# Kernel optimization log

Hardware: AMD Instinct MI355X
Metric: run time of the kernel (lower is better)

## Reference

```python
import jax, jax.numpy as jnp
import numpy as np

# Constants from mode='only_tv': gamma_l1=gamma_dwt=beta=lambda_l1=lambda_dwt=sigma=0,
# so u_l1,u_dwt,z,eta_l1,eta_dwt,rho stay identically zero and drop out of the math.
GAMMA_TV = 2.0
ALPHA = 5.0
LAMBDA_TV = 1e-4
N_ITER = 200


def soft_thresh(v, t):
    return jnp.sign(v) * jnp.maximum(jnp.abs(v) - t, 0.0)


def setup_inputs() -> dict:
    key = jax.random.key(0)
    k1, k2, k3 = jax.random.split(key, 3)
    target = jax.random.normal(k1, (4096, 64), dtype=jnp.float32)  # B spectra of K bands
    A = jax.random.normal(k2, (9, 64), dtype=jnp.float32) * 0.1     # (M=9 channels, K=64 bands)
    x0 = jax.random.normal(k3, (4096, 64), dtype=jnp.float32)       # replaces randn_like(target)
    return {"target": target, "A": A, "x0": x0}


def reference(target, A, x0):
    # target, x0: (B, K) batch of per-sample length-K vectors; A: (M, K)
    K = A.shape[1]
    AT = A.T  # (K, M)
    I = jnp.eye(K, dtype=A.dtype)
    Delta = jnp.roll(I, 1, axis=1) - I          # (K, K)
    DtD = Delta.T @ Delta
    inv_item = jnp.linalg.inv(AT @ A + GAMMA_TV * DtD + ALPHA * I)  # (K, K)

    # b = A @ x  per sample  ->  (B, M);  AT @ b per sample -> (B, K)
    b = target @ A.T
    ATb = b @ A

    # per-sample Delta @ v, batched over rows -> v_mat @ Delta.T
    def D(v):
        return v @ Delta.T

    eta_tv0 = jnp.zeros_like(x0)
    tau0 = jnp.zeros_like(x0)

    def step(carry, _):
        x, eta_tv, tau = carry
        u_tv = soft_thresh(D(x) + eta_tv / GAMMA_TV, LAMBDA_TV / GAMMA_TV)
        w = jnp.maximum(x + tau / ALPHA, 0.0)
        # note: torch's matmul(z_tv, DeltaT) on a vector equals Delta @ z_tv -> batched D(.)
        resid = ATb + D(GAMMA_TV * u_tv - eta_tv) + ALPHA * w - tau
        x = resid @ inv_item.T  # per-sample inv_item @ resid
        eta_tv = eta_tv + GAMMA_TV * (D(x) - u_tv)
        tau = tau + ALPHA * (x - w)
        return (x, eta_tv, tau), None

    (x, _, _), _ = jax.lax.scan(step, (x0, eta_tv0, tau0), None, length=N_ITER)
    return x
```

## Files before the change

### kernel.cpp

```cpp
#include <hip/hip_runtime.h>

#define NSAMP 4096
#define NITER 200

#define DPL(op, acc, rr, mm, rot) \
  op " " acc ", " rr ", " mm " row_ror:" #rot " row_mask:0xf bank_mask:0xf\n\t"

__global__ __launch_bounds__(256)
void admm_fused(const float* __restrict__ target, const float* __restrict__ A,
                const float* __restrict__ x0, float* __restrict__ out) {
  __shared__ __align__(16) char smem[39952];
  float (*Mfull)[64] = (float(*)[64])(smem);
  float* Mperm       = (float*)(smem + 16384);
  float (*rbuf)[64]  = (float(*)[64])(smem + 32768);
  double* lamr       = (double*)(smem + 32768);
  float* binv        = (float*)(smem + 33792);
  float (*P)[64]     = (float(*)[64])(smem + 34048);
  float (*Q)[64]     = (float(*)[64])(smem + 36352);
  double (*W)[18]    = (double(*)[18])(smem + 38656);

  const int tid = threadIdx.x;
  const int wid = tid >> 6;
  const int lane = tid & 63;
  const int s = blockIdx.x * 4 + wid;
  const double TWO_PI = 6.283185307179586476925286766559;

  double cb = 0.0;
  if (tid < 64) {
    cb = cos(TWO_PI * (double)tid / 64.0);
    lamr[tid] = 1.0 / (9.0 - 4.0 * cb);
  }
  __syncthreads();
  if (tid < 64) {
    double cm1 = 1.0, c0 = cb;
    double acc = lamr[0] + cb * lamr[1];
#pragma unroll 16
    for (int m = 2; m < 64; ++m) {
      double c = 2.0 * cb * c0 - cm1;
      cm1 = c0;
      c0 = c;
      acc += c * lamr[m];
    }
    binv[tid] = (float)(acc / 64.0);
  }
  __syncthreads();

  for (int e = tid; e < 9 * 64; e += 256) {
    int m = e >> 6, i = e & 63;
    double acc = 0.0;
#pragma unroll 16
    for (int k = 0; k < 64; ++k)
      acc += (double)A[m * 64 + k] * (double)binv[(k - i) & 63];
    P[m][i] = (float)acc;
  }
  __syncthreads();

  if (tid < 81) {
    int m = tid / 9, n = tid % 9;
    double acc = (m == n) ? 1.0 : 0.0;
#pragma unroll 16
    for (int i = 0; i < 64; ++i)
      acc += (double)P[m][i] * (double)A[n * 64 + i];
    W[m][n] = acc;
    W[m][n + 9] = (m == n) ? 1.0 : 0.0;
  }
  __syncthreads();

  {
    const int r9 = tid / 18, c9 = tid % 18;
    const bool act = (tid < 162);
    for (int k = 0; k < 9; ++k) {
      double pv = 1.0, f = 0.0, wkc = 0.0;
      if (act) {
        pv = W[k][k];
        f = W[r9][k];
        wkc = W[k][c9];
      }
      __syncthreads();
      if (act) {
        double nk = wkc / pv;
        W[r9][c9] = (r9 == k) ? nk : fma(-f, nk, W[r9][c9]);
      }
      __syncthreads();
    }
  }

  for (int e = tid; e < 9 * 64; e += 256) {
    int m = e >> 6, j = e & 63;
    double acc = 0.0;
#pragma unroll
    for (int n = 0; n < 9; ++n) acc += W[m][n + 9] * (double)P[n][j];
    Q[m][j] = (float)acc;
  }
  __syncthreads();

  for (int e = tid; e < 64 * 64; e += 256) {
    int i = e >> 6, j = e & 63;
    float acc = binv[(i - j) & 63];
#pragma unroll
    for (int m = 0; m < 9; ++m) acc = fmaf(-P[m][i], Q[m][j], acc);
    Mfull[i][j] = acc;
  }
  __syncthreads();

  int dpp1;
  asm volatile(
      "s_nop 4\n\t"
      "v_mov_b32_dpp %0, %1 row_ror:1 row_mask:0xf bank_mask:0xf\n\t"
      "s_nop 4"
      : "=v"(dpp1)
      : "v"(lane));
  const int dir = (__builtin_amdgcn_readfirstlane(dpp1) == 1) ? 1 : -1;

  for (int e = tid; e < 64 * 64; e += 256) {
    int li = e >> 6, k = e & 63;
    int j;
    if (k < 32) {
      int t = k & 15;
      int q = (li & 48) | (((li & 15) + dir * t + 16) & 15);
      j = (k < 16) ? q : (q ^ 16);
    } else {
      j = ((li & 32) ^ 32) + (k - 32);
    }
    Mperm[li * 64 + k] = Mfull[li][j];
  }
  __syncthreads();

  float t = target[s * 64 + lane];
  float atbv = 0.f;
#pragma unroll
  for (int m = 0; m < 9; ++m) {
    float a = A[m * 64 + lane];
    float p = t * a;
#pragma unroll
    for (int off = 32; off; off >>= 1) p += __shfl_xor(p, off, 64);
    atbv = fmaf(a, p, atbv);
  }

  unsigned int mprm = (unsigned int)(uintptr_t)(Mperm + lane * 64);
  unsigned int rb = (unsigned int)(uintptr_t)(&rbuf[wid][0]);
  unsigned int a_w = rb + lane * 4;
  unsigned int a_rf = rb + (((lane & 32) ^ 32) << 2);
  unsigned int a_nxt = ((lane + 1) & 63) * 4;
  float xin = x0[s * 64 + lane];
  float xout;
  int cnt_s;
  const int smask = 0x7fffffff;
  const float sthr = 5e-5f, sc02 = 0.2f, sc5 = 5.0f;

  asm volatile(
      "s_mov_b32 m0, -1\n\t"
      "ds_read_b128 v[64:67],   %[mprm]\n\t"
      "ds_read_b128 v[68:71],   %[mprm] offset:16\n\t"
      "ds_read_b128 v[72:75],   %[mprm] offset:32\n\t"
      "ds_read_b128 v[76:79],   %[mprm] offset:48\n\t"
      "ds_read_b128 v[80:83],   %[mprm] offset:64\n\t"
      "ds_read_b128 v[84:87],   %[mprm] offset:80\n\t"
      "ds_read_b128 v[88:91],   %[mprm] offset:96\n\t"
      "ds_read_b128 v[92:95],   %[mprm] offset:112\n\t"
      "ds_read_b128 v[96:99],   %[mprm] offset:128\n\t"
      "ds_read_b128 v[100:103], %[mprm] offset:144\n\t"
      "ds_read_b128 v[104:107], %[mprm] offset:160\n\t"
      "ds_read_b128 v[108:111], %[mprm] offset:176\n\t"
      "ds_read_b128 v[112:115], %[mprm] offset:192\n\t"
      "ds_read_b128 v[116:119], %[mprm] offset:208\n\t"
      "ds_read_b128 v[120:123], %[mprm] offset:224\n\t"
      "ds_read_b128 v[124:127], %[mprm] offset:240\n\t"
      "v_mov_b32 v32, %[xin]\n\t"
      "v_mov_b32 v36, %[atb]\n\t"
      "v_mov_b32 v33, 0\n\t"
      "v_mov_b32 v34, 0\n\t"
      "ds_bpermute_b32 v45, %[anx], v32\n\t"
      "s_waitcnt lgkmcnt(0)\n\t"
      "v_sub_f32 v35, v45, v32\n\t"
      "s_movk_i32 %[cnt], 200\n\t"
      "1:\n\t"
      "v_fma_f32 v40, 0.5, v33, v35\n\t"
      "v_and_b32 v41, %[msk], v40\n\t"
      "v_subrev_f32 v41, %[thr], v41\n\t"
      "v_max_f32 v41, 0, v41\n\t"
      "v_bfi_b32 v42, %[msk], v41, v40\n\t"
      "v_fma_f32 v43, %[c02], v34, v32\n\t"
      "v_max_f32 v43, 0, v43\n\t"
      "v_fma_f32 v40, 2.0, v42, -v33\n\t"
      "ds_bpermute_b32 v45, %[anx], v40\n\t"
      "v_fma_f32 v44, %[c5], v43, v36\n\t"
      "v_sub_f32 v44, v44, v34\n\t"
      "v_sub_f32 v44, v44, v40\n\t"
      "s_waitcnt lgkmcnt(0)\n\t"
      "v_add_f32 v44, v44, v45\n\t"
      "ds_write_b32 %[aw], v44\n\t"
      "ds_swizzle_b32 v47, v44 offset:0x401F\n\t"
      "ds_read_b128 v[48:51], %[arf]\n\t"
      "ds_read_b128 v[52:55], %[arf] offset:16\n\t"
      "ds_read_b128 v[56:59], %[arf] offset:32\n\t"
      "ds_read_b128 v[60:63], %[arf] offset:48\n\t"
      "ds_read_b128 v[16:19], %[arf] offset:64\n\t"
      "ds_read_b128 v[20:23], %[arf] offset:80\n\t"
      "ds_read_b128 v[24:27], %[arf] offset:96\n\t"
      "ds_read_b128 v[28:31], %[arf] offset:112\n\t"
      "v_mul_f32 v37, v44, v64\n\t"
      DPL("v_mul_f32",  "v38", "v44", "v65", 1)
      DPL("v_mul_f32",  "v39", "v44", "v66", 2)
      DPL("v_mul_f32",  "v40", "v44", "v67", 3)
      DPL("v_fmac_f32", "v37", "v44", "v68", 4)
      DPL("v_fmac_f32", "v38", "v44", "v69", 5)
      DPL("v_fmac_f32", "v39", "v44", "v70", 6)
      DPL("v_fmac_f32", "v40", "v44", "v71", 7)
      DPL("v_fmac_f32", "v37", "v44", "v72", 8)
      DPL("v_fmac_f32", "v38", "v44", "v73", 9)
      DPL("v_fmac_f32", "v39", "v44", "v74", 10)
      DPL("v_fmac_f32", "v40", "v44", "v75", 11)
      DPL("v_fmac_f32", "v37", "v44", "v76", 12)
      DPL("v_fmac_f32", "v38", "v44", "v77", 13)
      DPL("v_fmac_f32", "v39", "v44", "v78", 14)
      DPL("v_fmac_f32", "v40", "v44", "v79", 15)
      "s_waitcnt lgkmcnt(8)\n\t"
      "s_nop 1\n\t"
      "v_fmac_f32 v37, v47, v80\n\t"
      DPL("v_fmac_f32", "v38", "v47", "v81", 1)
      DPL("v_fmac_f32", "v39", "v47", "v82", 2)
      DPL("v_fmac_f32", "v40", "v47", "v83", 3)
      DPL("v_fmac_f32", "v37", "v47", "v84", 4)
      DPL("v_fmac_f32", "v38", "v47", "v85", 5)
      DPL("v_fmac_f32", "v39", "v47", "v86", 6)
      DPL("v_fmac_f32", "v40", "v47", "v87", 7)
      DPL("v_fmac_f32", "v37", "v47", "v88", 8)
      DPL("v_fmac_f32", "v38", "v47", "v89", 9)
      DPL("v_fmac_f32", "v39", "v47", "v90", 10)
      DPL("v_fmac_f32", "v40", "v47", "v91", 11)
      DPL("v_fmac_f32", "v37", "v47", "v92", 12)
      DPL("v_fmac_f32", "v38", "v47", "v93", 13)
      DPL("v_fmac_f32", "v39", "v47", "v94", 14)
      DPL("v_fmac_f32", "v40", "v47", "v95", 15)
      "s_waitcnt lgkmcnt(4)\n\t"
      "v_fmac_f32 v37, v48, v96\n\t"
      "v_fmac_f32 v38, v49, v97\n\t"
      "v_fmac_f32 v39, v50, v98\n\t"
      "v_fmac_f32 v40, v51, v99\n\t"
      "v_fmac_f32 v37, v52, v100\n\t"
      "v_fmac_f32 v38, v53, v101\n\t"
      "v_fmac_f32 v39, v54, v102\n\t"
      "v_fmac_f32 v40, v55, v103\n\t"
      "v_fmac_f32 v37, v56, v104\n\t"
      "v_fmac_f32 v38, v57, v105\n\t"
      "v_fmac_f32 v39, v58, v106\n\t"
      "v_fmac_f32 v40, v59, v107\n\t"
      "v_fmac_f32 v37, v60, v108\n\t"
      "v_fmac_f32 v38, v61, v109\n\t"
      "v_fmac_f32 v39, v62, v110\n\t"
      "v_fmac_f32 v40, v63, v111\n\t"
      "s_waitcnt lgkmcnt(0)\n\t"
      "v_fmac_f32 v37, v16, v112\n\t"
      "v_fmac_f32 v38, v17, v113\n\t"
      "v_fmac_f32 v39, v18, v114\n\t"
      "v_fmac_f32 v40, v19, v115\n\t"
      "v_fmac_f32 v37, v20, v116\n\t"
      "v_fmac_f32 v38, v21, v117\n\t"
      "v_fmac_f32 v39, v22, v118\n\t"
      "v_fmac_f32 v40, v23, v119\n\t"
      "v_fmac_f32 v37, v24, v120\n\t"
      "v_fmac_f32 v38, v25, v121\n\t"
      "v_fmac_f32 v39, v26, v122\n\t"
      "v_fmac_f32 v40, v27, v123\n\t"
      "v_fmac_f32 v37, v28, v124\n\t"
      "v_fmac_f32 v38, v29, v125\n\t"
      "v_fmac_f32 v39, v30, v126\n\t"
      "v_fmac_f32 v40, v31, v127\n\t"
      "v_add_f32 v37, v37, v38\n\t"
      "v_add_f32 v39, v39, v40\n\t"
      "v_add_f32 v32, v37, v39\n\t"
      "ds_bpermute_b32 v45, %[anx], v32\n\t"
      "v_sub_f32 v41, v32, v43\n\t"
      "v_fma_f32 v34, %[c5], v41, v34\n\t"
      "s_waitcnt lgkmcnt(0)\n\t"
      "v_sub_f32 v35, v45, v32\n\t"
      "v_sub_f32 v41, v35, v42\n\t"
      "v_fma_f32 v33, 2.0, v41, v33\n\t"
      "s_sub_u32 %[cnt], %[cnt], 1\n\t"
      "s_cmp_lg_u32 %[cnt], 0\n\t"
      "s_cbranch_scc1 1b\n\t"
      "v_mov_b32 %[xout], v32\n\t"
      : [xout] "=v"(xout), [cnt] "=&s"(cnt_s)
      : [mprm] "v"(mprm), [aw] "v"(a_w), [arf] "v"(a_rf), [anx] "v"(a_nxt),
        [xin] "v"(xin), [atb] "v"(atbv),
        [msk] "s"(smask), [thr] "s"(sthr), [c02] "s"(sc02), [c5] "s"(sc5)
      : "memory", "scc",
        "v16","v17","v18","v19","v20","v21","v22","v23","v24","v25","v26","v27",
        "v28","v29","v30","v31",
        "v32","v33","v34","v35","v36","v37","v38","v39","v40","v41","v42","v43",
        "v44","v45","v46","v47","v48","v49","v50","v51","v52","v53","v54","v55",
        "v56","v57","v58","v59","v60","v61","v62","v63","v64","v65","v66","v67",
        "v68","v69","v70","v71","v72","v73","v74","v75","v76","v77","v78","v79",
        "v80","v81","v82","v83","v84","v85","v86","v87","v88","v89","v90","v91",
        "v92","v93","v94","v95","v96","v97","v98","v99","v100","v101","v102",
        "v103","v104","v105","v106","v107","v108","v109","v110","v111","v112",
        "v113","v114","v115","v116","v117","v118","v119","v120","v121","v122",
        "v123","v124","v125","v126","v127");

  out[s * 64 + lane] = xout;
}

extern "C" void kernel_launch(void* const* d_in, const int* in_sizes, int n_in,
                              void* d_out, int out_size, void* d_ws, size_t ws_size,
                              hipStream_t stream) {
  const float* target = (const float*)d_in[0];
  const float* A = (const float*)d_in[1];
  const float* x0 = (const float*)d_in[2];
  float* out = (float*)d_out;

  admm_fused<<<NSAMP / 4, 256, 0, stream>>>(target, A, x0, out);
}
```

Measured before the change: 187.4 us.

## Rebuild prologue inverse setup in vectorized fp32 and write padded Mperm directly

The per-block construction of the 64x64 iteration matrix changes from scalar double-precision loops to vectorized fp32 dot products. It uses shifted copies of the circulant inverse and a duplicated A. The Mfull intermediate is dropped: each thread computes 16 entries in registers and scatters them straight into the permuted layout, and the smaller LDS footprint may allow more resident blocks. Mperm rows are padded to stride 65 to reduce bank conflicts. This risks fp32 accuracy loss in the 9x9 Gauss-Jordan inverse, and the 260-byte row stride breaks the 16-byte alignment assumed by the ds_read_b128 loads.

After: 203.1 us. 1.08x slower.

```diff
diff --git a/kernel.cpp b/kernel.cpp
--- a/kernel.cpp
+++ b/kernel.cpp
@@ -9,21 +9,31 @@
 __global__ __launch_bounds__(256)
 void admm_fused(const float* __restrict__ target, const float* __restrict__ A,
                 const float* __restrict__ x0, float* __restrict__ out) {
-  __shared__ __align__(16) char smem[39952];
-  float (*Mfull)[64] = (float(*)[64])(smem);
-  float* Mperm       = (float*)(smem + 16384);
-  float (*rbuf)[64]  = (float(*)[64])(smem + 32768);
-  double* lamr       = (double*)(smem + 32768);
-  float* binv        = (float*)(smem + 33792);
-  float (*P)[64]     = (float(*)[64])(smem + 34048);
-  float (*Q)[64]     = (float(*)[64])(smem + 36352);
-  double (*W)[18]    = (double(*)[18])(smem + 38656);
+  __shared__ __align__(16) char smem[30704];
+  float* Mperm      = (float*)(smem);
+  float (*rbuf)[64] = (float(*)[64])(smem + 16640);
+  double* lamr      = (double*)(smem + 16640);
+  float* binv       = (float*)(smem + 17664);
+  float* binvN      = (float*)(smem + 17920);
+  float (*binvS)[68]= (float(*)[68])(smem + 18176);
+  float (*bnS)[80]  = (float(*)[80])(smem + 19264);
+  float (*As2)[128] = (float(*)[128])(smem + 20544);
+  float (*P)[68]    = (float(*)[68])(smem + 25152);
+  float (*Q)[68]    = (float(*)[68])(smem + 27600);
+  float (*W)[18]    = (float(*)[18])(smem + 30048);
 
   const int tid = threadIdx.x;
   const int wid = tid >> 6;
   const int lane = tid & 63;
   const int s = blockIdx.x * 4 + wid;
   const double TWO_PI = 6.283185307179586476925286766559;
+
+  for (int e = tid; e < 9 * 64; e += 256) {
+    int m = e >> 6, k = e & 63;
+    float a = A[e];
+    As2[m][k] = a;
+    As2[m][k + 64] = a;
+  }
 
   double cb = 0.0;
   if (tid < 64) {
@@ -41,28 +51,57 @@
       c0 = c;
       acc += c * lamr[m];
     }
-    binv[tid] = (float)(acc / 64.0);
-  }
-  __syncthreads();
-
-  for (int e = tid; e < 9 * 64; e += 256) {
-    int m = e >> 6, i = e & 63;
-    double acc = 0.0;
-#pragma unroll 16
-    for (int k = 0; k < 64; ++k)
-      acc += (double)A[m * 64 + k] * (double)binv[(k - i) & 63];
-    P[m][i] = (float)acc;
+    float b = (float)(acc / 64.0);
+    binv[tid] = b;
+    binvN[(64 - tid) & 63] = b;
+  }
+  __syncthreads();
+
+  for (int e = tid; e < 4 * 68; e += 256) {
+    int sh = e / 68, d = e % 68;
+    binvS[sh][d] = (d >= sh && d < 64 + sh) ? binv[d - sh] : 0.f;
+  }
+  for (int e = tid; e < 4 * 80; e += 256) {
+    int sh = e / 80, d = e % 80;
+    bnS[sh][d] = binvN[(d - sh) & 63];
+  }
+  __syncthreads();
+
+  {
+    int w = wid, i = lane;
+    int ia = i & ~3, sh = i & 3;
+    for (int m = w; m < 9; m += 4) {
+      const float4* ap = (const float4*)&As2[m][ia];
+      const float4* bp = (const float4*)&binvS[sh][0];
+      float acc = 0.f;
+#pragma unroll
+      for (int t = 0; t < 17; ++t) {
+        float4 av = ap[t], bv = bp[t];
+        acc = fmaf(av.x, bv.x, acc);
+        acc = fmaf(av.y, bv.y, acc);
+        acc = fmaf(av.z, bv.z, acc);
+        acc = fmaf(av.w, bv.w, acc);
+      }
+      P[m][i] = acc;
+    }
   }
   __syncthreads();
 
   if (tid < 81) {
     int m = tid / 9, n = tid % 9;
-    double acc = (m == n) ? 1.0 : 0.0;
-#pragma unroll 16
-    for (int i = 0; i < 64; ++i)
-      acc += (double)P[m][i] * (double)A[n * 64 + i];
+    float acc = (m == n) ? 1.f : 0.f;
+    const float4* pp = (const float4*)&P[m][0];
+    const float4* aa = (const float4*)&As2[n][0];
+#pragma unroll
+    for (int q = 0; q < 16; ++q) {
+      float4 pv = pp[q], av = aa[q];
+      acc = fmaf(pv.x, av.x, acc);
+      acc = fmaf(pv.y, av.y, acc);
+      acc = fmaf(pv.z, av.z, acc);
+      acc = fmaf(pv.w, av.w, acc);
+    }
     W[m][n] = acc;
-    W[m][n + 9] = (m == n) ? 1.0 : 0.0;
+    W[m][n + 9] = (m == n) ? 1.f : 0.f;
   }
   __syncthreads();
 
@@ -70,7 +109,7 @@
     const int r9 = tid / 18, c9 = tid % 18;
     const bool act = (tid < 162);
     for (int k = 0; k < 9; ++k) {
-      double pv = 1.0, f = 0.0, wkc = 0.0;
+      float pv = 1.f, f = 0.f, wkc = 0.f;
       if (act) {
         pv = W[k][k];
         f = W[r9][k];
@@ -78,28 +117,26 @@
       }
       __syncthreads();
       if (act) {
-        double nk = wkc / pv;
-        W[r9][c9] = (r9 == k) ? nk : fma(-f, nk, W[r9][c9]);
+        float nk = wkc / pv;
+        W[r9][c9] = (r9 == k) ? nk : fmaf(-f, nk, W[r9][c9]);
       }
       __syncthreads();
     }
   }
 
-  for (int e = tid; e < 9 * 64; e += 256) {
-    int m = e >> 6, j = e & 63;
-    double acc = 0.0;
-#pragma unroll
-    for (int n = 0; n < 9; ++n) acc += W[m][n + 9] * (double)P[n][j];
-    Q[m][j] = (float)acc;
-  }
-  __syncthreads();
-
-  for (int e = tid; e < 64 * 64; e += 256) {
-    int i = e >> 6, j = e & 63;
-    float acc = binv[(i - j) & 63];
-#pragma unroll
-    for (int m = 0; m < 9; ++m) acc = fmaf(-P[m][i], Q[m][j], acc);
-    Mfull[i][j] = acc;
+  if (tid < 144) {
+    int m = tid >> 4, jq = tid & 15;
+    float4 acc = {0.f, 0.f, 0.f, 0.f};
+#pragma unroll
+    for (int n = 0; n < 9; ++n) {
+      float sv = W[m][n + 9];
+      float4 pv = *(const float4*)&P[n][4 * jq];
+      acc.x = fmaf(sv, pv.x, acc.x);
+      acc.y = fmaf(sv, pv.y, acc.y);
+      acc.z = fmaf(sv, pv.z, acc.z);
+      acc.w = fmaf(sv, pv.w, acc.w);
+    }
+    *(float4*)&Q[m][4 * jq] = acc;
   }
   __syncthreads();
 
@@ -112,17 +149,49 @@
       : "v"(lane));
   const int dir = (__builtin_amdgcn_readfirstlane(dpp1) == 1) ? 1 : -1;
 
-  for (int e = tid; e < 64 * 64; e += 256) {
-    int li = e >> 6, k = e & 63;
-    int j;
-    if (k < 32) {
-      int t = k & 15;
-      int q = (li & 48) | (((li & 15) + dir * t + 16) & 15);
-      j = (k < 16) ? q : (q ^ 16);
-    } else {
-      j = ((li & 32) ^ 32) + (k - 32);
-    }
-    Mperm[li * 64 + k] = Mfull[li][j];
+  {
+    int i = tid >> 2, jb = tid & 3, j0 = jb * 16;
+    int sh = i & 3;
+    float pm[9];
+#pragma unroll
+    for (int m = 0; m < 9; ++m) pm[m] = P[m][i];
+
+    float vq[16];
+    {
+      int b = (j0 - (i & ~3)) & 63;
+      const float4* bq = (const float4*)&bnS[sh][b];
+      float4 b0 = bq[0], b1 = bq[1], b2 = bq[2], b3 = bq[3];
+      vq[0] = b0.x;  vq[1] = b0.y;  vq[2] = b0.z;  vq[3] = b0.w;
+      vq[4] = b1.x;  vq[5] = b1.y;  vq[6] = b1.z;  vq[7] = b1.w;
+      vq[8] = b2.x;  vq[9] = b2.y;  vq[10] = b2.z; vq[11] = b2.w;
+      vq[12] = b3.x; vq[13] = b3.y; vq[14] = b3.z; vq[15] = b3.w;
+    }
+#pragma unroll
+    for (int m = 0; m < 9; ++m) {
+      float p = pm[m];
+      const float4* qq = (const float4*)&Q[m][j0];
+      float4 q0 = qq[0], q1 = qq[1], q2 = qq[2], q3 = qq[3];
+      vq[0] = fmaf(-p, q0.x, vq[0]);   vq[1] = fmaf(-p, q0.y, vq[1]);
+      vq[2] = fmaf(-p, q0.z, vq[2]);   vq[3] = fmaf(-p, q0.w, vq[3]);
+      vq[4] = fmaf(-p, q1.x, vq[4]);   vq[5] = fmaf(-p, q1.y, vq[5]);
+      vq[6] = fmaf(-p, q1.z, vq[6]);   vq[7] = fmaf(-p, q1.w, vq[7]);
+      vq[8] = fmaf(-p, q2.x, vq[8]);   vq[9] = fmaf(-p, q2.y, vq[9]);
+      vq[10] = fmaf(-p, q2.z, vq[10]); vq[11] = fmaf(-p, q2.w, vq[11]);
+      vq[12] = fmaf(-p, q3.x, vq[12]); vq[13] = fmaf(-p, q3.y, vq[13]);
+      vq[14] = fmaf(-p, q3.z, vq[14]); vq[15] = fmaf(-p, q3.w, vq[15]);
+    }
+#pragma unroll
+    for (int e = 0; e < 16; ++e) {
+      int j = j0 + e;
+      int k;
+      if ((j ^ i) & 32) {
+        k = 32 + (j & 31);
+      } else {
+        int tt = (dir * ((j & 15) - (i & 15))) & 15;
+        k = ((j ^ i) & 16) ? 16 + tt : tt;
+      }
+      Mperm[i * 65 + k] = vq[e];
+    }
   }
   __syncthreads();
 
@@ -137,7 +206,7 @@
     atbv = fmaf(a, p, atbv);
   }
 
-  unsigned int mprm = (unsigned int)(uintptr_t)(Mperm + lane * 64);
+  unsigned int mprm = (unsigned int)(uintptr_t)(Mperm + lane * 65);
   unsigned int rb = (unsigned int)(uintptr_t)(&rbuf[wid][0]);
   unsigned int a_w = rb + lane * 4;
   unsigned int a_rf = rb + (((lane & 32) ^ 32) << 2);
```
